# Performance work log

Measured on AMD Instinct MI355X. Metric: run time of the kernel, lower is better.

## Reference

```python
import jax, jax.numpy as jnp
import numpy as np

_EPSILON = 1e-6

def _sparsemax(z):
    # sparsemax along last axis. z: [b, m]
    z_sorted = -jnp.sort(-z, axis=-1)                       # descending sort
    m = z.shape[-1]
    k = jnp.arange(1, m + 1, dtype=z.dtype)                 # [m]
    z_cumsum = jnp.cumsum(z_sorted, axis=-1)                # [b, m]
    support = (1.0 + k * z_sorted) > z_cumsum               # [b, m] bool
    k_z = jnp.sum(support, axis=-1, keepdims=True)          # [b, 1] int, size of support
    cs_at_k = jnp.take_along_axis(z_cumsum, k_z - 1, axis=-1)
    tau = (cs_at_k - 1.0) / k_z.astype(z.dtype)             # threshold
    return jnp.maximum(z - tau, 0.0)


def setup_inputs() -> dict:
    key = jax.random.key(0)
    ks = jax.random.split(key, 6)
    b, m, dim, out_dim = 4096, 8192, 1024, 1000
    encoder_output = jax.random.normal(ks[0], (b, dim), dtype=jnp.float32)
    memory_set = jax.random.normal(ks[1], (m, dim), dtype=jnp.float32)
    loss_weights = jax.random.uniform(ks[2], (m, 1), dtype=jnp.float32)
    # classifier: Linear(2*dim, 4*dim) -> ReLU -> Linear(4*dim, out_dim)
    W1 = jax.random.normal(ks[3], (4 * dim, 2 * dim), dtype=jnp.float32) * (1.0 / np.sqrt(2 * dim))
    b1 = jnp.zeros((4 * dim,), dtype=jnp.float32)
    W2 = jax.random.normal(ks[4], (out_dim, 4 * dim), dtype=jnp.float32) * (1.0 / np.sqrt(4 * dim))
    b2 = jnp.zeros((out_dim,), dtype=jnp.float32)
    return {"encoder_output": encoder_output, "memory_set": memory_set,
            "loss_weights": loss_weights, "W1": W1, "b1": b1, "W2": W2, "b2": b2}


def reference(encoder_output, memory_set, loss_weights, W1, b1, W2, b2):
    # cosine distance: d = 1 - x_norm @ y_norm^T
    x_norm = encoder_output * jax.lax.rsqrt(
        jnp.sum(encoder_output * encoder_output, axis=1, keepdims=True) + _EPSILON)
    y_norm = memory_set * jax.lax.rsqrt(
        jnp.sum(memory_set * memory_set, axis=1, keepdims=True) + _EPSILON)
    d = 1.0 - jnp.matmul(x_norm, y_norm.T)                  # [b, m]
    content_weights = _sparsemax(-d)                        # [b, m], sparse rows
    memory_vector = jnp.matmul(content_weights, memory_set) # [b, dim]
    final_input = jnp.concatenate([encoder_output, memory_vector], axis=1)  # [b, 2*dim]
    h = jax.nn.relu(jnp.matmul(final_input, W1.T) + b1)
    output = jnp.matmul(h, W2.T) + b2                       # [b, out_dim]
    return output
```

## Files before the change

### kernel.cpp

```cpp
#include <hip/hip_runtime.h>

typedef __bf16 bf16;
typedef __bf16 bf16x4 __attribute__((ext_vector_type(4)));
typedef __bf16 bf16x8 __attribute__((ext_vector_type(8)));
typedef float f32x4 __attribute__((ext_vector_type(4)));
typedef _Float16 f16x8 __attribute__((ext_vector_type(8)));

#define WS_OFF_S    (0ull)
#define WS_OFF_P4   (67108864ull)
#define WS_OFF_MB   (134217728ull)
#define WS_OFF_W1B  (150994944ull)
#define WS_OFF_W2B  (167772160ull)
#define WS_OFF_FI   (176160768ull)
#define WS_OFF_XN   (192937984ull)
#define WS_OFF_YN   (201326592ull)
#define WS_OFF_H    (0ull)

__device__ __forceinline__ void gload_lds16(const void* g, void* l) {
  __builtin_amdgcn_global_load_lds(
      (const __attribute__((address_space(1))) void*)g,
      (__attribute__((address_space(3))) void*)l, 16, 0, 0);
}

template<int EPI>
__global__ __launch_bounds__(256)
void gemm_nt(const bf16* __restrict__ A, const bf16* __restrict__ B,
             void* __restrict__ Cout, const float* __restrict__ bias,
             int K, int ldab, int ldc)
{
  __shared__ alignas(16) bf16 As[128 * 64];
  __shared__ alignas(16) bf16 Bs[128 * 64];
  const int tid  = threadIdx.x;
  const int lane = tid & 63;
  const int wave = tid >> 6;
  const int wr = wave >> 1, wc = wave & 1;
  const int bm0 = blockIdx.y << 7;
  const int bn0 = blockIdx.x << 7;
  const int zc  = blockIdx.z;

  const int lr   = lane >> 3;
  const int lcb  = (lane & 7) << 4;
  const int scolb = lcb ^ (lr << 4);
  const int row0 = (wave << 5) + lr;
  const char* Ag = (const char*)(A + (size_t)(bm0 + row0) * ldab + (size_t)zc * K) + scolb;
  const char* Bg = (const char*)(B + (size_t)(bn0 + row0) * ldab + (size_t)zc * K) + scolb;
  char* Al = (char*)As + (wave << 12);
  char* Bl = (char*)Bs + (wave << 12);
  const size_t rstride8 = (size_t)16 * ldab;

  int offA[2][4], offB[2][4];
  const int kb = (lane >> 4) << 4;
#pragma unroll
  for (int m = 0; m < 4; ++m) {
    const int rA = (wr << 6) + (m << 4) + (lane & 15);
    const int rB = (wc << 6) + (m << 4) + (lane & 15);
#pragma unroll
    for (int ks = 0; ks < 2; ++ks) {
      offA[ks][m] = (rA << 7) + ((((ks << 6) + kb)) ^ ((rA & 7) << 4));
      offB[ks][m] = (rB << 7) + ((((ks << 6) + kb)) ^ ((rB & 7) << 4));
    }
  }

  f32x4 acc[4][4];
#pragma unroll
  for (int m = 0; m < 4; ++m)
#pragma unroll
    for (int n = 0; n < 4; ++n) acc[m][n] = (f32x4)(0.0f);

  const char* Asb = (const char*)As;
  const char* Bsb = (const char*)Bs;
  const int nk = K >> 6;
  for (int kt = 0; kt < nk; ++kt) {
#pragma unroll
    for (int i = 0; i < 4; ++i) gload_lds16(Ag + i * rstride8, Al + (i << 10));
#pragma unroll
    for (int i = 0; i < 4; ++i) gload_lds16(Bg + i * rstride8, Bl + (i << 10));
    Ag += 128; Bg += 128;
    __syncthreads();
#pragma unroll
    for (int ks = 0; ks < 2; ++ks) {
      bf16x8 av[4], bv[4];
#pragma unroll
      for (int m = 0; m < 4; ++m) av[m] = *(const bf16x8*)(Asb + offA[ks][m]);
#pragma unroll
      for (int n = 0; n < 4; ++n) bv[n] = *(const bf16x8*)(Bsb + offB[ks][n]);
#pragma unroll
      for (int m = 0; m < 4; ++m)
#pragma unroll
        for (int n = 0; n < 4; ++n)
          acc[m][n] = __builtin_amdgcn_mfma_f32_16x16x32_bf16(av[m], bv[n], acc[m][n], 0, 0, 0);
    }
    __syncthreads();
  }

  const int r0 = bm0 + (wr << 6) + ((lane >> 4) << 2);
  const int c0 = bn0 + (wc << 6) + (lane & 15);
#pragma unroll
  for (int m = 0; m < 4; ++m) {
#pragma unroll
    for (int n = 0; n < 4; ++n) {
      const int col = c0 + (n << 4);
#pragma unroll
      for (int j = 0; j < 4; ++j) {
        const int row = r0 + (m << 4) + j;
        const float v = acc[m][n][j];
        if (EPI == 0) {
          ((_Float16*)Cout)[(size_t)row * ldc + col] = (_Float16)v;
        } else if (EPI == 2) {
          float t = v + bias[col];
          t = t > 0.f ? t : 0.f;
          ((bf16*)Cout)[(size_t)row * ldc + col] = (bf16)t;
        } else {
          ((float*)Cout)[((size_t)zc << 22) + (size_t)row * ldc + col] = v;
        }
      }
    }
  }
}

__global__ __launch_bounds__(256)
void reduce_bias_kernel(const float* __restrict__ P4, const float* __restrict__ b2,
                        float* __restrict__ out)
{
  const int row = blockIdx.x;
  const int t = threadIdx.x;
  if (t >= 250) return;
  const size_t base = (size_t)row * 1024 + (t << 2);
  const float4 p0 = *(const float4*)(P4 + base);
  const float4 p1 = *(const float4*)(P4 + base + (1ull << 22));
  const float4 p2 = *(const float4*)(P4 + base + (2ull << 22));
  const float4 p3 = *(const float4*)(P4 + base + (3ull << 22));
  const float4 bb = ((const float4*)b2)[t];
  float4 r;
  r.x = p0.x + p1.x + p2.x + p3.x + bb.x;
  r.y = p0.y + p1.y + p2.y + p3.y + bb.y;
  r.z = p0.z + p1.z + p2.z + p3.z + bb.z;
  r.w = p0.w + p1.w + p2.w + p3.w + bb.w;
  *(float4*)(out + (size_t)row * 1000 + (t << 2)) = r;
}

__global__ __launch_bounds__(256)
void rownorm_kernel(const float* __restrict__ X, bf16* __restrict__ XN,
                    bf16* __restrict__ RAW, int ldraw)
{
  const int row = blockIdx.x;
  const int tid = threadIdx.x;
  const float4 v = ((const float4*)(X + (size_t)row * 1024))[tid];
  float ss = v.x * v.x + v.y * v.y + v.z * v.z + v.w * v.w;
#pragma unroll
  for (int o = 32; o > 0; o >>= 1) ss += __shfl_down(ss, o);
  __shared__ float red[4];
  if ((tid & 63) == 0) red[tid >> 6] = ss;
  __syncthreads();
  const float rn = rsqrtf(red[0] + red[1] + red[2] + red[3] + 1e-6f);
  union { bf16 h[4]; unsigned long long u; } p;
  p.h[0] = (bf16)(v.x * rn); p.h[1] = (bf16)(v.y * rn);
  p.h[2] = (bf16)(v.z * rn); p.h[3] = (bf16)(v.w * rn);
  ((unsigned long long*)(XN + (size_t)row * 1024))[tid] = p.u;
  if (RAW != nullptr) {
    union { bf16 h[4]; unsigned long long u; } q;
    q.h[0] = (bf16)v.x; q.h[1] = (bf16)v.y; q.h[2] = (bf16)v.z; q.h[3] = (bf16)v.w;
    ((unsigned long long*)(RAW + (size_t)row * ldraw))[tid] = q.u;
  }
}

__global__ void cvt_bf16_kernel(const float* __restrict__ src, bf16* __restrict__ dst, int n4) {
  const int i = blockIdx.x * blockDim.x + threadIdx.x;
  if (i >= n4) return;
  const float4 v = ((const float4*)src)[i];
  union { bf16 h[4]; unsigned long long u; } p;
  p.h[0] = (bf16)v.x; p.h[1] = (bf16)v.y; p.h[2] = (bf16)v.z; p.h[3] = (bf16)v.w;
  ((unsigned long long*)dst)[i] = p.u;
}

__global__ void cvt_w2_kernel(const float* __restrict__ src, bf16* __restrict__ dst) {
  const int i = blockIdx.x * blockDim.x + threadIdx.x;
  const int row = i >> 10;
  union { bf16 h[4]; unsigned long long u; } p;
  if (row < 1000) {
    const float4 v = ((const float4*)src)[i];
    p.h[0] = (bf16)v.x; p.h[1] = (bf16)v.y; p.h[2] = (bf16)v.z; p.h[3] = (bf16)v.w;
  } else {
    p.u = 0ull;
  }
  ((unsigned long long*)dst)[i] = p.u;
}

#define LCAP 1024
__global__ __launch_bounds__(256)
void sparsemax_gather_kernel(const _Float16* __restrict__ S, const bf16* __restrict__ MB,
                             bf16* __restrict__ FI)
{
  const int row = blockIdx.x;
  const int tid = threadIdx.x;
  const f16x8* zs = (const f16x8*)(S + (size_t)row * 8192);
  float z[32];
  float lsum = 0.f;
#pragma unroll
  for (int t = 0; t < 4; ++t) {
    const f16x8 v = zs[t * 256 + tid];
#pragma unroll
    for (int j = 0; j < 8; ++j) { const float f = (float)v[j]; z[t * 8 + j] = f; lsum += f; }
  }
  __shared__ float redS[4], redC[4];
  __shared__ unsigned pbuf[LCAP];
  __shared__ int lcnt;
  float s = lsum;
#pragma unroll
  for (int o = 32; o > 0; o >>= 1) s += __shfl_down(s, o);
  if ((tid & 63) == 0) redS[tid >> 6] = s;
  __syncthreads();
  float tau = (redS[0] + redS[1] + redS[2] + redS[3] - 1.0f) * (1.0f / 8192.0f);

  for (int it = 0; it < 64; ++it) {
    float ls = 0.f, lc = 0.f;
#pragma unroll
    for (int j = 0; j < 32; ++j) {
      const float v = z[j];
      if (v > tau) { ls += v; lc += 1.0f; }
    }
#pragma unroll
    for (int o = 32; o > 0; o >>= 1) { ls += __shfl_down(ls, o); lc += __shfl_down(lc, o); }
    __syncthreads();
    if ((tid & 63) == 0) { redS[tid >> 6] = ls; redC[tid >> 6] = lc; }
    __syncthreads();
    const float Ssum = redS[0] + redS[1] + redS[2] + redS[3];
    const float Csum = redC[0] + redC[1] + redC[2] + redC[3];
    const float ntau = (Ssum - 1.0f) / Csum;
    if (!(ntau > tau)) break;
    tau = ntau;
  }

  unsigned pend = 0;
#pragma unroll
  for (int j = 0; j < 32; ++j)
    if (z[j] > tau) pend |= (1u << j);

  float4 acc = make_float4(0.f, 0.f, 0.f, 0.f);
  for (;;) {
    if (tid == 0) lcnt = 0;
    __syncthreads();
    unsigned rem = pend;
    while (rem) {
      const int j = __ffs(rem) - 1;
      rem &= rem - 1;
      const int slot = atomicAdd(&lcnt, 1);
      if (slot < LCAP) {
        union { _Float16 h; unsigned short us; } cv; cv.h = (_Float16)(z[j] - tau);
        const unsigned idx = (unsigned)(((j >> 3) * 256 + tid) * 8 + (j & 7));
        pbuf[slot] = ((unsigned)cv.us << 16) | idx;
        pend &= ~(1u << j);
      }
    }
    __syncthreads();
    const int nb = min(lcnt, LCAP);
    for (int e = 0; e < nb; ++e) {
      const unsigned pk = pbuf[e];
      union { unsigned short us; _Float16 h; } cv; cv.us = (unsigned short)(pk >> 16);
      const float w = (float)cv.h;
      const size_t idx = (size_t)(pk & 0xffffu);
      const bf16x4 v = ((const bf16x4*)(MB + (idx << 10)))[tid];
      acc.x += w * (float)v[0];
      acc.y += w * (float)v[1];
      acc.z += w * (float)v[2];
      acc.w += w * (float)v[3];
    }
    if (!__syncthreads_or(pend != 0)) break;
  }

  union { bf16 h[4]; unsigned long long u; } p;
  p.h[0] = (bf16)acc.x; p.h[1] = (bf16)acc.y; p.h[2] = (bf16)acc.z; p.h[3] = (bf16)acc.w;
  ((unsigned long long*)(FI + (size_t)row * 2048 + 1024))[tid] = p.u;
}

extern "C" void kernel_launch(void* const* d_in, const int* in_sizes, int n_in,
                              void* d_out, int out_size, void* d_ws, size_t ws_size,
                              hipStream_t stream)
{
  const float* enc = (const float*)d_in[0];
  const float* mem = (const float*)d_in[1];
  const float* W1  = (const float*)d_in[3];
  const float* b1  = (const float*)d_in[4];
  const float* W2  = (const float*)d_in[5];
  const float* b2  = (const float*)d_in[6];
  float* out = (float*)d_out;
  char* ws = (char*)d_ws;

  _Float16* S = (_Float16*)(ws + WS_OFF_S);
  float* P4 = (float*)(ws + WS_OFF_P4);
  bf16* MB  = (bf16*)(ws + WS_OFF_MB);
  bf16* W1B = (bf16*)(ws + WS_OFF_W1B);
  bf16* W2B = (bf16*)(ws + WS_OFF_W2B);
  bf16* FI  = (bf16*)(ws + WS_OFF_FI);
  bf16* XN  = (bf16*)(ws + WS_OFF_XN);
  bf16* YN  = (bf16*)(ws + WS_OFF_YN);
  bf16* H   = (bf16*)(ws + WS_OFF_H);

  rownorm_kernel<<<4096, 256, 0, stream>>>(enc, XN, FI, 2048);
  rownorm_kernel<<<8192, 256, 0, stream>>>(mem, YN, MB, 1024);
  cvt_bf16_kernel<<<8192, 256, 0, stream>>>(W1, W1B, 2097152);
  cvt_w2_kernel<<<4096, 256, 0, stream>>>(W2, W2B);

  gemm_nt<0><<<dim3(64, 32), 256, 0, stream>>>(XN, YN, S, nullptr, 1024, 1024, 8192);
  sparsemax_gather_kernel<<<4096, 256, 0, stream>>>(S, MB, FI);
  gemm_nt<2><<<dim3(32, 32), 256, 0, stream>>>(FI, W1B, H, b1, 2048, 2048, 4096);
  gemm_nt<4><<<dim3(8, 32, 4), 256, 0, stream>>>(H, W2B, P4, nullptr, 1024, 4096, 1024);
  reduce_bias_kernel<<<4096, 256, 0, stream>>>(P4, b2, out);
}
```

Before: 468.4 us.

## Use 256x256 GEMM tiles with double-buffered LDS prefetch across all GEMMs

Replaces the 128x128, 4-wave GEMM with a 256x256, 8-wave variant. It double-buffers the LDS tiles so global-to-LDS loads for tile t+2 overlap the MFMA work on tile t, using explicit vmcnt waits and raised wave priority during compute. Larger tiles raise arithmetic intensity and cut global traffic per FLOP. The cost is 128KB of LDS per block and far fewer blocks (e.g. 256 for the W2 GEMM), which may underfill the CUs.

```diff
diff --git a/kernel.cpp b/kernel.cpp
--- a/kernel.cpp
+++ b/kernel.cpp
@@ -23,80 +23,98 @@
 }
 
 template<int EPI>
-__global__ __launch_bounds__(256)
-void gemm_nt(const bf16* __restrict__ A, const bf16* __restrict__ B,
-             void* __restrict__ Cout, const float* __restrict__ bias,
-             int K, int ldab, int ldc)
-{
-  __shared__ alignas(16) bf16 As[128 * 64];
-  __shared__ alignas(16) bf16 Bs[128 * 64];
+__global__ __launch_bounds__(512, 2)
+void gemm_nt256(const bf16* __restrict__ A, const bf16* __restrict__ B,
+                void* __restrict__ Cout, const float* __restrict__ bias,
+                int K, int ldab, int ldc)
+{
+  __shared__ alignas(16) bf16 As[2][256 * 64];
+  __shared__ alignas(16) bf16 Bs[2][256 * 64];
   const int tid  = threadIdx.x;
   const int lane = tid & 63;
   const int wave = tid >> 6;
-  const int wr = wave >> 1, wc = wave & 1;
-  const int bm0 = blockIdx.y << 7;
-  const int bn0 = blockIdx.x << 7;
+  const int wr = wave >> 2, wc = wave & 3;
+  const int bm0 = blockIdx.y << 8;
+  const int bn0 = blockIdx.x << 8;
   const int zc  = blockIdx.z;
 
-  const int lr   = lane >> 3;
-  const int lcb  = (lane & 7) << 4;
-  const int scolb = lcb ^ (lr << 4);
-  const int row0 = (wave << 5) + lr;
+  const int lr    = lane >> 3;
+  const int scolb = ((lane & 7) << 4) ^ (lr << 4);
+  const int row0  = (wave << 5) + lr;
   const char* Ag = (const char*)(A + (size_t)(bm0 + row0) * ldab + (size_t)zc * K) + scolb;
   const char* Bg = (const char*)(B + (size_t)(bn0 + row0) * ldab + (size_t)zc * K) + scolb;
-  char* Al = (char*)As + (wave << 12);
-  char* Bl = (char*)Bs + (wave << 12);
+  char* Alds = (char*)As + (wave << 12);
+  char* Blds = (char*)Bs + (wave << 12);
   const size_t rstride8 = (size_t)16 * ldab;
 
-  int offA[2][4], offB[2][4];
+  int offA[2][8], offB[2][4];
   const int kb = (lane >> 4) << 4;
 #pragma unroll
-  for (int m = 0; m < 4; ++m) {
-    const int rA = (wr << 6) + (m << 4) + (lane & 15);
-    const int rB = (wc << 6) + (m << 4) + (lane & 15);
+  for (int ks = 0; ks < 2; ++ks) {
+#pragma unroll
+    for (int m = 0; m < 8; ++m) {
+      const int rA = (wr << 7) + (m << 4) + (lane & 15);
+      offA[ks][m] = (rA << 7) + ((((ks << 6) + kb)) ^ ((rA & 7) << 4));
+    }
+#pragma unroll
+    for (int n = 0; n < 4; ++n) {
+      const int rB = (wc << 6) + (n << 4) + (lane & 15);
+      offB[ks][n] = (rB << 7) + ((((ks << 6) + kb)) ^ ((rB & 7) << 4));
+    }
+  }
+
+  f32x4 acc[8][4];
+#pragma unroll
+  for (int m = 0; m < 8; ++m)
+#pragma unroll
+    for (int n = 0; n < 4; ++n) acc[m][n] = (f32x4)(0.0f);
+
+  auto STAGE = [&](int buf) {
+    char* Ad = Alds + (buf << 15);
+    char* Bd = Blds + (buf << 15);
+#pragma unroll
+    for (int i = 0; i < 4; ++i) gload_lds16(Ag + i * rstride8, Ad + (i << 10));
+#pragma unroll
+    for (int i = 0; i < 4; ++i) gload_lds16(Bg + i * rstride8, Bd + (i << 10));
+    Ag += 128; Bg += 128;
+  };
+
+  const int nt = K >> 6;
+  STAGE(0);
+  STAGE(1);
+  int cur = 0;
+  for (int t = 0; t < nt; ++t) {
+    if (t + 1 < nt) { asm volatile("s_waitcnt vmcnt(8)" ::: "memory"); }
+    else            { asm volatile("s_waitcnt vmcnt(0)" ::: "memory"); }
+    __builtin_amdgcn_s_barrier();
+    asm volatile("" ::: "memory");
+    const char* Ab = (const char*)As + (cur << 15);
+    const char* Bb = (const char*)Bs + (cur << 15);
+    __builtin_amdgcn_s_setprio(1);
 #pragma unroll
     for (int ks = 0; ks < 2; ++ks) {
-      offA[ks][m] = (rA << 7) + ((((ks << 6) + kb)) ^ ((rA & 7) << 4));
-      offB[ks][m] = (rB << 7) + ((((ks << 6) + kb)) ^ ((rB & 7) << 4));
-    }
-  }
-
-  f32x4 acc[4][4];
-#pragma unroll
-  for (int m = 0; m < 4; ++m)
-#pragma unroll
-    for (int n = 0; n < 4; ++n) acc[m][n] = (f32x4)(0.0f);
-
-  const char* Asb = (const char*)As;
-  const char* Bsb = (const char*)Bs;
-  const int nk = K >> 6;
-  for (int kt = 0; kt < nk; ++kt) {
-#pragma unroll
-    for (int i = 0; i < 4; ++i) gload_lds16(Ag + i * rstride8, Al + (i << 10));
-#pragma unroll
-    for (int i = 0; i < 4; ++i) gload_lds16(Bg + i * rstride8, Bl + (i << 10));
-    Ag += 128; Bg += 128;
-    __syncthreads();
-#pragma unroll
-    for (int ks = 0; ks < 2; ++ks) {
-      bf16x8 av[4], bv[4];
-#pragma unroll
-      for (int m = 0; m < 4; ++m) av[m] = *(const bf16x8*)(Asb + offA[ks][m]);
-#pragma unroll
-      for (int n = 0; n < 4; ++n) bv[n] = *(const bf16x8*)(Bsb + offB[ks][n]);
-#pragma unroll
-      for (int m = 0; m < 4; ++m)
+      bf16x8 av[8], bv[4];
+#pragma unroll
+      for (int m = 0; m < 8; ++m) av[m] = *(const bf16x8*)(Ab + offA[ks][m]);
+#pragma unroll
+      for (int n = 0; n < 4; ++n) bv[n] = *(const bf16x8*)(Bb + offB[ks][n]);
+#pragma unroll
+      for (int m = 0; m < 8; ++m)
 #pragma unroll
         for (int n = 0; n < 4; ++n)
           acc[m][n] = __builtin_amdgcn_mfma_f32_16x16x32_bf16(av[m], bv[n], acc[m][n], 0, 0, 0);
     }
-    __syncthreads();
-  }
-
-  const int r0 = bm0 + (wr << 6) + ((lane >> 4) << 2);
+    __builtin_amdgcn_s_setprio(0);
+    asm volatile("" ::: "memory");
+    __builtin_amdgcn_s_barrier();
+    if (t + 2 < nt) STAGE(cur);
+    cur ^= 1;
+  }
+
+  const int r0 = bm0 + (wr << 7) + ((lane >> 4) << 2);
   const int c0 = bn0 + (wc << 6) + (lane & 15);
 #pragma unroll
-  for (int m = 0; m < 4; ++m) {
+  for (int m = 0; m < 8; ++m) {
 #pragma unroll
     for (int n = 0; n < 4; ++n) {
       const int col = c0 + (n << 4);
@@ -107,9 +125,9 @@
         if (EPI == 0) {
           ((_Float16*)Cout)[(size_t)row * ldc + col] = (_Float16)v;
         } else if (EPI == 2) {
-          float t = v + bias[col];
-          t = t > 0.f ? t : 0.f;
-          ((bf16*)Cout)[(size_t)row * ldc + col] = (bf16)t;
+          float t2 = v + bias[col];
+          t2 = t2 > 0.f ? t2 : 0.f;
+          ((bf16*)Cout)[(size_t)row * ldc + col] = (bf16)t2;
         } else {
           ((float*)Cout)[((size_t)zc << 22) + (size_t)row * ldc + col] = v;
         }
@@ -301,9 +319,9 @@
   cvt_bf16_kernel<<<8192, 256, 0, stream>>>(W1, W1B, 2097152);
   cvt_w2_kernel<<<4096, 256, 0, stream>>>(W2, W2B);
 
-  gemm_nt<0><<<dim3(64, 32), 256, 0, stream>>>(XN, YN, S, nullptr, 1024, 1024, 8192);
+  gemm_nt256<0><<<dim3(32, 16), 512, 0, stream>>>(XN, YN, S, nullptr, 1024, 1024, 8192);
   sparsemax_gather_kernel<<<4096, 256, 0, stream>>>(S, MB, FI);
-  gemm_nt<2><<<dim3(32, 32), 256, 0, stream>>>(FI, W1B, H, b1, 2048, 2048, 4096);
-  gemm_nt<4><<<dim3(8, 32, 4), 256, 0, stream>>>(H, W2B, P4, nullptr, 1024, 4096, 1024);
+  gemm_nt256<2><<<dim3(16, 16), 512, 0, stream>>>(FI, W1B, H, b1, 2048, 2048, 4096);
+  gemm_nt256<4><<<dim3(4, 16, 4), 512, 0, stream>>>(H, W2B, P4, nullptr, 1024, 4096, 1024);
   reduce_bias_kernel<<<4096, 256, 0, stream>>>(P4, b2, out);
 }
```

After: 449.7 us. 1.04x faster.
